# Performance work log

Hardware: AMD Instinct MI355X
Metric: run time of the kernel (lower is better)

Reference implementation:

```python
import jax, jax.numpy as jnp
import numpy as np

NUM_EMB = 1000
HIDDEN = 256
SCALE = 2
N_HEADS = 8
HEAD_DIM = HIDDEN * SCALE // N_HEADS  # 64
HS = HIDDEN * SCALE  # 512
EPS = 1e-6


def setup_inputs() -> dict:
    key = jax.random.key(0)
    ks = jax.random.split(key, 12)
    B, N, C, H, W = 8, 8, HIDDEN, 32, 32
    std = 0.02
    return {
        "q": jax.random.randint(ks[0], (B,), 0, NUM_EMB, dtype=jnp.int32),
        "c": jax.random.normal(ks[1], (B, N, C, H, W), dtype=jnp.float32),
        "rms_w": jnp.ones((HIDDEN,), dtype=jnp.float32),
        "emb": jax.random.normal(ks[2], (NUM_EMB, HIDDEN), dtype=jnp.float32) * std,
        "w1": jax.random.normal(ks[3], (HIDDEN, HS), dtype=jnp.float32) * std,
        "b1": jnp.zeros((HS,), dtype=jnp.float32),
        "w2": jax.random.normal(ks[4], (HS, HS), dtype=jnp.float32) * std,
        "b2": jnp.zeros((HS,), dtype=jnp.float32),
        "w_kv": jax.random.normal(ks[5], (HIDDEN, HS * 2), dtype=jnp.float32) * std,
        "w_out": jax.random.normal(ks[6], (HS, HIDDEN), dtype=jnp.float32) * std,
        "b_out": jnp.zeros((HIDDEN,), dtype=jnp.float32),
    }


def reference(q, c, rms_w, emb, w1, b1, w2, b2, w_kv, w_out, b_out):
    B, N, C, H, W = c.shape
    attn_scale = HEAD_DIM ** (-0.5)
    # permute to [B,H,W,N,C] and RMSNorm over channel dim
    c = jnp.transpose(c, (0, 3, 4, 1, 2))
    c = c * jax.lax.rsqrt(jnp.mean(c * c, axis=-1, keepdims=True) + EPS) * rms_w
    # query path: embed + gated MLP -> [B, n_heads, head_dim]
    qe = emb[q]                                   # [B, hidden]
    qh = jax.nn.silu(qe @ w1 + b1) @ w2 + b2      # [B, HS]
    qh = qh.reshape(B, N_HEADS, HEAD_DIM)
    # kv projection: [B,H,W,N, 2*HS] -> [B,H,W,n_heads,N, 2*head_dim]
    kv = (c @ w_kv).reshape(B, H, W, N, N_HEADS, 2 * HEAD_DIM)
    kv = jnp.transpose(kv, (0, 1, 2, 4, 3, 5))
    k, v = jnp.split(kv, 2, axis=-1)              # each [B,H,W,heads,N,head_dim]
    # broadcast per-pixel cross-attention: query shared over H,W
    dots = jnp.einsum('bed,bhwend->bhwen', qh, k) * attn_scale
    attn = jax.nn.softmax(dots, axis=-1)
    h = jnp.einsum('bhwen,bhwend->bhwed', attn, v)  # [B,H,W,heads,head_dim]
    h = h.reshape(B, H, W, HS)
    out = h @ w_out + b_out                        # [B,H,W,hidden]
    return jnp.transpose(out, (0, 3, 1, 2))        # [B,hidden,H,W]
```

## Files before the change

kernel.cpp:

```cpp
#include <hip/hip_runtime.h>

typedef _Float16 f16;
typedef _Float16 f16x4 __attribute__((ext_vector_type(4)));
typedef _Float16 f16x8 __attribute__((ext_vector_type(8)));
typedef float f32x4 __attribute__((ext_vector_type(4)));

static __device__ inline char* a_addr(char* Abase, int px, int k) {
    return Abase + px * 4096 + ((((k >> 3) ^ (px & 15)) << 4) | ((k & 7) << 1));
}

__launch_bounds__(1024)
__global__ void k_setup(const int* __restrict__ q, const float* __restrict__ emb,
                        const float* __restrict__ w1, const float* __restrict__ b1,
                        const float* __restrict__ w2, const float* __restrict__ b2,
                        const float* __restrict__ w_kv, const float* __restrict__ w_out,
                        const float* __restrict__ rms_w,
                        f16* __restrict__ qkw, f16* __restrict__ mtp) {
    int blk = blockIdx.x;
    int t = threadIdx.x;

    if (blk < 8) {
        int b = blk;
        __shared__ float qe[256];
        __shared__ float x1[512];
        __shared__ float qh[512];
        __shared__ float psA[1024];
        __shared__ float psB[1024];

        if (t < 256) qe[t] = emb[(size_t)q[b] * 256 + t];
        __syncthreads();

        {
            int h = t & 511, half = t >> 9;
            float acc = half ? 0.f : b1[h];
            int c0 = half * 128;
#pragma unroll 8
            for (int c = c0; c < c0 + 128; ++c)
                acc += qe[c] * w1[(size_t)c * 512 + h];
            psA[half * 512 + h] = acc;
        }
        __syncthreads();
        if (t < 512) {
            float a = psA[t] + psA[512 + t];
            x1[t] = a / (1.f + __expf(-a));
        }
        __syncthreads();

        {
            int o = t & 511, half = t >> 9;
            float acc = half ? 0.f : b2[o];
            int k0 = half * 256;
#pragma unroll 8
            for (int k = k0; k < k0 + 256; ++k)
                acc += x1[k] * w2[(size_t)k * 512 + o];
            psB[half * 512 + o] = acc;
        }
        __syncthreads();
        if (t < 512) qh[t] = psB[t] + psB[512 + t];
        __syncthreads();

        {
            int c = t & 255, g = t >> 8;
            float rw = rms_w[c];
#pragma unroll
            for (int ee = 0; ee < 2; ++ee) {
                int e = g * 2 + ee;
                const float* col = w_kv + (size_t)c * 1024 + e * 128;
                float acc = 0.f;
#pragma unroll
                for (int dq = 0; dq < 16; ++dq) {
                    float4 wv4 = *(const float4*)(col + dq * 4);
                    const float* qb = &qh[e * 64 + dq * 4];
                    acc += wv4.x * qb[0] + wv4.y * qb[1]
                         + wv4.z * qb[2] + wv4.w * qb[3];
                }
                qkw[((size_t)b * 8 + e) * 256 + c] = (f16)(acc * rw);
            }
        }
    } else {
        __shared__ float wv[4][64][8];
        int sub = t >> 8, st = t & 255;
        int mb = (blk - 8) * 4 + sub;
        int e = mb >> 5, c0 = (mb & 31) * 8;
        {
            int d = st & 63, cc = st >> 6;
            wv[sub][d][cc]     = w_kv[(size_t)(c0 + cc) * 1024 + e * 128 + 64 + d];
            wv[sub][d][cc + 4] = w_kv[(size_t)(c0 + cc + 4) * 1024 + e * 128 + 64 + d];
        }
        __syncthreads();
        int o = st;
        float acc[8];
#pragma unroll
        for (int c = 0; c < 8; ++c) acc[c] = 0.f;
#pragma unroll 4
        for (int d = 0; d < 64; ++d) {
            float wo = w_out[(size_t)(e * 64 + d) * 256 + o];
            float4 wa = *(const float4*)&wv[sub][d][0];
            float4 wb = *(const float4*)&wv[sub][d][4];
            acc[0] += wa.x * wo; acc[1] += wa.y * wo; acc[2] += wa.z * wo; acc[3] += wa.w * wo;
            acc[4] += wb.x * wo; acc[5] += wb.y * wo; acc[6] += wb.z * wo; acc[7] += wb.w * wo;
        }
        f16x8 ov;
#pragma unroll
        for (int c = 0; c < 8; ++c) ov[c] = (f16)(acc[c] * rms_w[c0 + c]);
        *(f16x8*)(mtp + ((size_t)((e * 256 + c0) >> 3) * 256 + o) * 8) = ov;
    }
}

__launch_bounds__(1024, 4)
__global__ void k_attn(const float* __restrict__ cin, const f16* __restrict__ qkw,
                       const f16* __restrict__ mtp, const float* __restrict__ b_out,
                       float* __restrict__ out) {
    int blk = blockIdx.x;
    int b = blk & 7;
    int hw0 = (blk >> 3) * 32;
    int t = threadIdx.x;
    int lane = t & 63, w = t >> 6;
    int m16 = lane & 15, quad = lane >> 4;
    int half = lane >> 5;

    __shared__ char A[32 * 4096];
    __shared__ float dotsP[8][8][32];
    __shared__ char pool[16384];
    __shared__ float rinvL[32][8];

    float* wredF = (float*)pool;
    f16*   attnH = (f16*)pool;

    int px = lane & 31;
    int cb = w + half * 16;
    const float* cbase = cin + ((size_t)b * 8 * 256) * 1024 + hw0 + px;
#pragma unroll
    for (int g = 0; g < 8; g += 2) {
        const float* s0 = cbase + ((size_t)(g * 256 + cb * 8) << 10);
        const float* s1 = cbase + ((size_t)((g + 1) * 256 + cb * 8) << 10);
        float v0[8], v1[8];
#pragma unroll
        for (int j = 0; j < 8; ++j) v0[j] = s0[(size_t)j << 10];
#pragma unroll
        for (int j = 0; j < 8; ++j) v1[j] = s1[(size_t)j << 10];
        float sa = 0.f, sb = 0.f;
        f16x8 h0, h1;
#pragma unroll
        for (int j = 0; j < 8; ++j) { sa += v0[j] * v0[j]; h0[j] = (f16)v0[j]; }
#pragma unroll
        for (int j = 0; j < 8; ++j) { sb += v1[j] * v1[j]; h1[j] = (f16)v1[j]; }
        *(f16x8*)a_addr(A, px, g * 256 + cb * 8)       = h0;
        *(f16x8*)a_addr(A, px, (g + 1) * 256 + cb * 8) = h1;
        sa += __shfl_xor(sa, 32);
        sb += __shfl_xor(sb, 32);
        if (lane < 32) {
            wredF[w * 256 + g * 32 + px]       = sa;
            wredF[w * 256 + (g + 1) * 32 + px] = sb;
        }
    }
    __syncthreads();

    if (t < 256) {
        int p = t >> 3, n = t & 7;
        float ss = 0.f;
#pragma unroll
        for (int ww = 0; ww < 16; ++ww) ss += wredF[ww * 256 + n * 32 + p];
        rinvL[p][n] = rsqrtf(ss * (1.f / 256.f) + 1e-6f);
    }
    {
        int n = w & 7, pxh = w >> 3;
        f32x4 d0 = {0.f, 0.f, 0.f, 0.f};
        const f16* qrow = qkw + (size_t)b * 2048 + (m16 & 7) * 256;
#pragma unroll
        for (int ks = 0; ks < 8; ++ks) {
            f16x8 a0  = *(const f16x8*)a_addr(A, pxh * 16 + m16, n * 256 + ks * 32 + quad * 8);
            f16x8 bfr = *(const f16x8*)(qrow + ks * 32 + quad * 8);
            d0 = __builtin_amdgcn_mfma_f32_16x16x32_f16(a0, bfr, d0, 0, 0, 0);
        }
        if (m16 < 8) {
#pragma unroll
            for (int r = 0; r < 4; ++r) dotsP[n][m16][pxh * 16 + quad * 4 + r] = d0[r];
        }
    }
    __syncthreads();

    int o = w * 16 + m16;
    f16x8 pb[8];
#pragma unroll
    for (int ks = 0; ks < 8; ++ks)
        pb[ks] = *(const f16x8*)(mtp + ((size_t)(ks * 4 + quad) * 256 + o) * 8);

    if (t < 256) {
        int e = t >> 5, p = t & 31;
        float rv[8], l[8];
#pragma unroll
        for (int n = 0; n < 8; ++n) rv[n] = rinvL[p][n];
#pragma unroll
        for (int n = 0; n < 8; ++n) l[n] = dotsP[n][e][p] * rv[n] * 0.125f;
        float mx = l[0];
#pragma unroll
        for (int n = 1; n < 8; ++n) mx = fmaxf(mx, l[n]);
        float s = 0.f;
#pragma unroll
        for (int n = 0; n < 8; ++n) { l[n] = __expf(l[n] - mx); s += l[n]; }
        float inv = 1.f / s;
        f16x8 av;
#pragma unroll
        for (int n = 0; n < 8; ++n) av[n] = (f16)(l[n] * inv * rv[n]);
        *(f16x8*)(attnH + e * 256 + p * 8) = av;
    }
    __syncthreads();

    {
        int bpx = lane & 31;
        int c0 = (w + half * 16) * 8;
        f16x8 cv[8];
#pragma unroll
        for (int n = 0; n < 8; ++n)
            cv[n] = *(const f16x8*)a_addr(A, bpx, n * 256 + c0);
#pragma unroll
        for (int e = 0; e < 8; ++e) {
            f16x8 av = *(const f16x8*)(attnH + e * 256 + bpx * 8);
            f16x8 r = {};
#pragma unroll
            for (int n = 0; n < 8; ++n) {
                f16 an = av[n];
#pragma unroll
                for (int j = 0; j < 8; ++j) r[j] += cv[n][j] * an;
            }
            *(f16x8*)a_addr(A, bpx, e * 256 + c0) = r;
        }
    }
    __syncthreads();

    {
        f32x4 acc0 = {0.f, 0.f, 0.f, 0.f};
        f32x4 acc1 = {0.f, 0.f, 0.f, 0.f};
#pragma unroll
        for (int ks = 0; ks < 8; ++ks) {
            int k = ks * 32 + quad * 8;
            f16x8 af0 = *(const f16x8*)a_addr(A, m16, k);
            f16x8 af1 = *(const f16x8*)a_addr(A, m16 + 16, k);
            acc0 = __builtin_amdgcn_mfma_f32_16x16x32_f16(af0, pb[ks], acc0, 0, 0, 0);
            acc1 = __builtin_amdgcn_mfma_f32_16x16x32_f16(af1, pb[ks], acc1, 0, 0, 0);
        }
#pragma unroll 8
        for (int ks = 8; ks < 64; ++ks) {
            int k = (ks >> 3) * 256 + (ks & 7) * 32 + quad * 8;
            int kchunk = k >> 3;
            f16x8 bfr = *(const f16x8*)(mtp + ((size_t)kchunk * 256 + o) * 8);
            f16x8 af0 = *(const f16x8*)a_addr(A, m16, k);
            f16x8 af1 = *(const f16x8*)a_addr(A, m16 + 16, k);
            acc0 = __builtin_amdgcn_mfma_f32_16x16x32_f16(af0, bfr, acc0, 0, 0, 0);
            acc1 = __builtin_amdgcn_mfma_f32_16x16x32_f16(af1, bfr, acc1, 0, 0, 0);
        }
        float bo = b_out[o];
        float* drow = out + ((size_t)b * 256 + o) * 1024 + hw0;
        float4 v0 = {acc0[0] + bo, acc0[1] + bo, acc0[2] + bo, acc0[3] + bo};
        float4 v1 = {acc1[0] + bo, acc1[1] + bo, acc1[2] + bo, acc1[3] + bo};
        *(float4*)(drow + quad * 4)      = v0;
        *(float4*)(drow + 16 + quad * 4) = v1;
    }
}

extern "C" void kernel_launch(void* const* d_in, const int* in_sizes, int n_in,
                              void* d_out, int out_size, void* d_ws, size_t ws_size,
                              hipStream_t stream) {
    (void)in_sizes; (void)n_in; (void)out_size; (void)ws_size;
    const int*   q     = (const int*)d_in[0];
    const float* c     = (const float*)d_in[1];
    const float* rms_w = (const float*)d_in[2];
    const float* emb   = (const float*)d_in[3];
    const float* w1    = (const float*)d_in[4];
    const float* b1    = (const float*)d_in[5];
    const float* w2    = (const float*)d_in[6];
    const float* b2    = (const float*)d_in[7];
    const float* w_kv  = (const float*)d_in[8];
    const float* w_out = (const float*)d_in[9];
    const float* b_out = (const float*)d_in[10];
    float* out = (float*)d_out;

    char* ws = (char*)d_ws;
    f16* qkw = (f16*)ws;
    f16* mtp = (f16*)(ws + 32768);

    k_setup<<<72, 1024, 0, stream>>>(q, emb, w1, b1, w2, b2, w_kv, w_out, rms_w, qkw, mtp);
    k_attn <<<256, 1024, 0, stream>>>(c, qkw, mtp, b_out, out);
}
```

Before: 171.8 us.

## Split query MLP across 96 blocks with atomic-flag inter-block dependencies

The query path (embedding, two MLP layers, qkw projection) previously ran in 8 serial blocks, one per batch. It now runs as three stages of 32 blocks each, with every block handling a slice of output columns for all batches. Stages exchange intermediates through global workspace and wait on atomic counters with acquire/release spin-waits. This shortens the serial critical path of the setup kernel. In exchange it adds a memset launch, global round-trips, and relies on all waiting blocks being co-resident, which risks deadlock if they are not.

New measurement: 191.4 us. 11.4% more time.

```diff
diff --git a/kernel.cpp b/kernel.cpp
--- a/kernel.cpp
+++ b/kernel.cpp
@@ -5,8 +5,28 @@
 typedef _Float16 f16x8 __attribute__((ext_vector_type(8)));
 typedef float f32x4 __attribute__((ext_vector_type(4)));
 
+#define WS_QKW   0
+#define WS_MTP   32768
+#define WS_FLAGS (32768 + 1048576)
+#define WS_X1    (WS_FLAGS + 128)
+#define WS_QH    (WS_X1 + 16384)
+
 static __device__ inline char* a_addr(char* Abase, int px, int k) {
     return Abase + px * 4096 + ((((k >> 3) ^ (px & 15)) << 4) | ((k & 7) << 1));
+}
+
+static __device__ inline void post_count(int* f) {
+    __threadfence();
+    __syncthreads();
+    if (threadIdx.x == 0)
+        __hip_atomic_fetch_add(f, 1, __ATOMIC_RELEASE, __HIP_MEMORY_SCOPE_AGENT);
+}
+static __device__ inline void wait_count(int* f, int target) {
+    if (threadIdx.x == 0) {
+        while (__hip_atomic_load(f, __ATOMIC_ACQUIRE, __HIP_MEMORY_SCOPE_AGENT) < target)
+            __builtin_amdgcn_s_sleep(8);
+    }
+    __syncthreads();
 }
 
 __launch_bounds__(1024)
@@ -15,72 +35,95 @@
                         const float* __restrict__ w2, const float* __restrict__ b2,
                         const float* __restrict__ w_kv, const float* __restrict__ w_out,
                         const float* __restrict__ rms_w,
-                        f16* __restrict__ qkw, f16* __restrict__ mtp) {
+                        f16* __restrict__ qkw, f16* __restrict__ mtp,
+                        float* __restrict__ x1g, float* __restrict__ qhg,
+                        int* __restrict__ flags) {
     int blk = blockIdx.x;
     int t = threadIdx.x;
 
-    if (blk < 8) {
-        int b = blk;
-        __shared__ float qe[256];
-        __shared__ float x1[512];
-        __shared__ float qh[512];
-        __shared__ float psA[1024];
-        __shared__ float psB[1024];
-
-        if (t < 256) qe[t] = emb[(size_t)q[b] * 256 + t];
-        __syncthreads();
-
+    if (blk < 32) {
+        __shared__ float qe[8][256];
+        __shared__ float ps[8][8][16];
+        int hs = blk * 16;
+        for (int i = t; i < 2048; i += 1024) {
+            int bb = i >> 8, c = i & 255;
+            qe[bb][c] = emb[(size_t)q[bb] * 256 + c];
+        }
+        __syncthreads();
         {
-            int h = t & 511, half = t >> 9;
-            float acc = half ? 0.f : b1[h];
-            int c0 = half * 128;
-#pragma unroll 8
-            for (int c = c0; c < c0 + 128; ++c)
-                acc += qe[c] * w1[(size_t)c * 512 + h];
-            psA[half * 512 + h] = acc;
-        }
-        __syncthreads();
-        if (t < 512) {
-            float a = psA[t] + psA[512 + t];
-            x1[t] = a / (1.f + __expf(-a));
-        }
-        __syncthreads();
-
+            int hl = t & 15, b = (t >> 4) & 7, qq = t >> 7;
+            int h = hs + hl;
+            float acc = 0.f;
+#pragma unroll
+            for (int c = qq * 32; c < qq * 32 + 32; ++c)
+                acc += qe[b][c] * w1[(size_t)c * 512 + h];
+            ps[qq][b][hl] = acc;
+        }
+        __syncthreads();
+        if (t < 128) {
+            int b = t >> 4, hl = t & 15;
+            float a = b1[hs + hl];
+#pragma unroll
+            for (int qq = 0; qq < 8; ++qq) a += ps[qq][b][hl];
+            x1g[b * 512 + hs + hl] = a / (1.f + __expf(-a));
+        }
+        post_count(&flags[0]);
+    } else if (blk < 64) {
+        __shared__ float x1L[8][512];
+        __shared__ float ps[8][8][16];
+        int os = (blk - 32) * 16;
+        wait_count(&flags[0], 32);
+        for (int i = t; i < 4096; i += 1024) {
+            int bb = i >> 9, k = i & 511;
+            x1L[bb][k] = x1g[bb * 512 + k];
+        }
+        __syncthreads();
         {
-            int o = t & 511, half = t >> 9;
-            float acc = half ? 0.f : b2[o];
-            int k0 = half * 256;
-#pragma unroll 8
-            for (int k = k0; k < k0 + 256; ++k)
-                acc += x1[k] * w2[(size_t)k * 512 + o];
-            psB[half * 512 + o] = acc;
-        }
-        __syncthreads();
-        if (t < 512) qh[t] = psB[t] + psB[512 + t];
-        __syncthreads();
-
-        {
-            int c = t & 255, g = t >> 8;
-            float rw = rms_w[c];
-#pragma unroll
-            for (int ee = 0; ee < 2; ++ee) {
-                int e = g * 2 + ee;
-                const float* col = w_kv + (size_t)c * 1024 + e * 128;
-                float acc = 0.f;
-#pragma unroll
-                for (int dq = 0; dq < 16; ++dq) {
-                    float4 wv4 = *(const float4*)(col + dq * 4);
-                    const float* qb = &qh[e * 64 + dq * 4];
-                    acc += wv4.x * qb[0] + wv4.y * qb[1]
-                         + wv4.z * qb[2] + wv4.w * qb[3];
-                }
-                qkw[((size_t)b * 8 + e) * 256 + c] = (f16)(acc * rw);
-            }
-        }
+            int ol = t & 15, b = (t >> 4) & 7, qq = t >> 7;
+            int o = os + ol;
+            float acc = 0.f;
+#pragma unroll 16
+            for (int k = qq * 64; k < qq * 64 + 64; ++k)
+                acc += x1L[b][k] * w2[(size_t)k * 512 + o];
+            ps[qq][b][ol] = acc;
+        }
+        __syncthreads();
+        if (t < 128) {
+            int b = t >> 4, ol = t & 15;
+            float a = b2[os + ol];
+#pragma unroll
+            for (int qq = 0; qq < 8; ++qq) a += ps[qq][b][ol];
+            qhg[b * 512 + os + ol] = a;
+        }
+        post_count(&flags[1]);
+    } else if (blk < 96) {
+        __shared__ float qhL[8][512];
+        __shared__ float ps2[512];
+        int cs = (blk - 64) * 8;
+        wait_count(&flags[1], 32);
+        for (int i = t; i < 4096; i += 1024) {
+            int bb = i >> 9, k = i & 511;
+            qhL[bb][k] = qhg[bb * 512 + k];
+        }
+        __syncthreads();
+        int cl = t & 7, e = (t >> 3) & 7, b = (t >> 6) & 7, dh = t >> 9;
+        int c = cs + cl;
+        const float* col = w_kv + (size_t)c * 1024 + e * 128 + dh * 32;
+        float acc = 0.f;
+#pragma unroll
+        for (int dq = 0; dq < 8; ++dq) {
+            float4 wv4 = *(const float4*)(col + dq * 4);
+            const float* qb = &qhL[b][e * 64 + dh * 32 + dq * 4];
+            acc += wv4.x * qb[0] + wv4.y * qb[1] + wv4.z * qb[2] + wv4.w * qb[3];
+        }
+        if (dh) ps2[t - 512] = acc;
+        __syncthreads();
+        if (t < 512)
+            qkw[((size_t)b * 8 + e) * 256 + c] = (f16)((acc + ps2[t]) * rms_w[c]);
     } else {
         __shared__ float wv[4][64][8];
         int sub = t >> 8, st = t & 255;
-        int mb = (blk - 8) * 4 + sub;
+        int mb = (blk - 96) * 4 + sub;
         int e = mb >> 5, c0 = (mb & 31) * 8;
         {
             int d = st & 63, cc = st >> 6;
@@ -277,9 +320,14 @@
     float* out = (float*)d_out;
 
     char* ws = (char*)d_ws;
-    f16* qkw = (f16*)ws;
-    f16* mtp = (f16*)(ws + 32768);
-
-    k_setup<<<72, 1024, 0, stream>>>(q, emb, w1, b1, w2, b2, w_kv, w_out, rms_w, qkw, mtp);
+    f16*   qkw   = (f16*)(ws + WS_QKW);
+    f16*   mtp   = (f16*)(ws + WS_MTP);
+    int*   flags = (int*)(ws + WS_FLAGS);
+    float* x1g   = (float*)(ws + WS_X1);
+    float* qhg   = (float*)(ws + WS_QH);
+
+    hipMemsetAsync(flags, 0, 64, stream);
+    k_setup<<<160, 1024, 0, stream>>>(q, emb, w1, b1, w2, b2, w_kv, w_out, rms_w,
+                                      qkw, mtp, x1g, qhg, flags);
     k_attn <<<256, 1024, 0, stream>>>(c, qkw, mtp, b_out, out);
 }
```
